# Performance work log

Hardware: AMD Instinct MI355X
Metric: run time of the kernel (lower is better)

Reference implementation:

```python
import jax, jax.numpy as jnp
import numpy as np

MAXHD = 100.0
MAXV = 40.0
LSTM_UNITS = 20
IN_DIM = 12


def setup_inputs() -> dict:
    key = jax.random.key(0)
    ks = jax.random.split(key, 10)
    nveh, nt = 8192, 512
    leadfol_inputs = jax.random.normal(ks[0], (nveh, nt, IN_DIM), dtype=jnp.float32)
    true_traj = jax.random.normal(ks[1], (nveh, nt), dtype=jnp.float32)
    hidden_states = jnp.zeros((2, nveh, LSTM_UNITS), dtype=jnp.float32)
    s = 0.1
    # LSTM kernel/recurrent kernel/bias (keras gate order: i, f, c, o)
    W_k = jax.random.normal(ks[2], (IN_DIM, 4 * LSTM_UNITS), dtype=jnp.float32) * s
    W_r = jax.random.normal(ks[3], (LSTM_UNITS, 4 * LSTM_UNITS), dtype=jnp.float32) * s
    b_l = jnp.zeros((4 * LSTM_UNITS,), dtype=jnp.float32)
    # dense (10, relu) and lc_actions (3)
    W_d = jax.random.normal(ks[4], (LSTM_UNITS, 10), dtype=jnp.float32) * s
    b_d = jnp.zeros((10,), dtype=jnp.float32)
    W_lc = jax.random.normal(ks[5], (10, 3), dtype=jnp.float32) * s
    b_lc = jnp.zeros((3,), dtype=jnp.float32)
    return {"leadfol_inputs": leadfol_inputs, "true_traj": true_traj,
            "hidden_states": hidden_states, "W_k": W_k, "W_r": W_r, "b_l": b_l,
            "W_d": W_d, "b_d": b_d, "W_lc": W_lc, "b_lc": b_lc}


def reference(leadfol_inputs, true_traj, hidden_states, W_k, W_r, b_l, W_d, b_d, W_lc, b_lc):
    # time-major for scan: (nt, nveh, ...)
    lf_t = jnp.swapaxes(leadfol_inputs, 0, 1)
    pos_t = jnp.swapaxes(true_traj, 0, 1)

    def step(carry, xt):
        h, c = carry
        pos, lf = xt  # pos: (nveh,), lf: (nveh, 12)
        lead_hd = (lf[:, :3] - pos[:, None]) / MAXHD
        fol_hd = (pos[:, None] - lf[:, 3:6]) / MAXHD
        spds = lf[:, 6:] / MAXV
        x = jnp.concatenate([lead_hd, fol_hd, spds], axis=1)
        x = jnp.where(jnp.isnan(x), jnp.ones_like(x), x)
        z = x @ W_k + h @ W_r + b_l
        zi, zf, zg, zo = jnp.split(z, 4, axis=1)
        c = jax.nn.sigmoid(zf) * c + jax.nn.sigmoid(zi) * jnp.tanh(zg)
        h = jax.nn.sigmoid(zo) * jnp.tanh(c)
        d = jax.nn.relu(h @ W_d + b_d)
        lc = d @ W_lc + b_lc
        return (h, c), lc

    (h, c), lc_t = jax.lax.scan(step, (hidden_states[0], hidden_states[1]), (pos_t, lf_t))
    pred_lc_action = jnp.swapaxes(lc_t, 0, 1)  # (nveh, nt, 3)
    return (true_traj, pred_lc_action, h, c)
```

## Files before the change

### kernel.cpp

```cpp
#include <hip/hip_runtime.h>

#define NVEH 8192
#define NT   512

typedef short bf16x8 __attribute__((ext_vector_type(8)));
typedef float f32x4  __attribute__((ext_vector_type(4)));

__device__ __forceinline__ float fsig(float x) {
    float e = __builtin_amdgcn_exp2f(-1.44269504f * x);
    return __builtin_amdgcn_rcpf(1.0f + e);
}
__device__ __forceinline__ float ftanh(float x) {
    float e = __builtin_amdgcn_exp2f(-2.88539008f * x);
    return 2.0f * __builtin_amdgcn_rcpf(1.0f + e) - 1.0f;
}
__device__ __forceinline__ unsigned short f2bf(float f) {
    union { float f; unsigned u; } vv; vv.f = f;
    unsigned r = vv.u + 0x7fff + ((vv.u >> 16) & 1);
    return (unsigned short)(r >> 16);
}

__device__ __forceinline__ void lds_barrier() {
    asm volatile("s_waitcnt lgkmcnt(0)" ::: "memory");
    __builtin_amdgcn_s_barrier();
    asm volatile("" ::: "memory");
}

__global__ __launch_bounds__(128) void lstm_scan_kernel(
    const float* __restrict__ lead, const float* __restrict__ traj,
    const float* __restrict__ hidden,
    const float* __restrict__ W_k, const float* __restrict__ W_r,
    const float* __restrict__ b_l, const float* __restrict__ W_d,
    const float* __restrict__ b_d, const float* __restrict__ W_lc,
    const float* __restrict__ b_lc,
    float* __restrict__ out_lc, float* __restrict__ out_h, float* __restrict__ out_c)
{
    __shared__ alignas(16) unsigned short row[2][16][40];

    const int tid  = threadIdx.x;
    const int wid  = tid >> 6;
    const int lane = tid & 63;
    const int q    = lane >> 4;
    const int v    = lane & 15;
    const int gv   = blockIdx.x * 16 + v;

    const int TTB = wid ? 3 : 0;

    bf16x8 aW[3]; f32x4 cB[3];
    #pragma unroll
    for (int l = 0; l < 3; ++l) {
        if (l < 2 || wid == 0) {
            const int tt = TTB + l;
            #pragma unroll
            for (int j = 0; j < 8; ++j) {
                int k = q * 8 + j;
                int p = 16 * tt + v;
                int u = p >> 2, g = p & 3;
                int col = g * 20 + u;
                float w = (k < 12) ? W_k[k * 80 + col] : W_r[(k - 12) * 80 + col];
                aW[l][j] = (short)f2bf(w);
            }
            #pragma unroll
            for (int reg = 0; reg < 4; ++reg)
                cB[l][reg] = b_l[reg * 20 + 4 * tt + q];
        }
    }

    bf16x8 aH = {};
    f32x4 cD = {};
    float wlc[4][3] = {};
    float pb0[3] = {};
    if (wid == 1) {
        #pragma unroll
        for (int j = 0; j < 8; ++j) {
            int k = q * 8 + j;
            aH[j] = (v < 10 && k >= 12) ? (short)f2bf(W_d[(k - 12) * 10 + v]) : (short)0;
        }
        #pragma unroll
        for (int reg = 0; reg < 4; ++reg) {
            int m = 4 * q + reg;
            cD[reg] = (m < 10) ? b_d[m] : 0.0f;
            #pragma unroll
            for (int j = 0; j < 3; ++j)
                wlc[reg][j] = (m < 10) ? W_lc[m * 3 + j] : 0.0f;
        }
        #pragma unroll
        for (int j = 0; j < 3; ++j) pb0[j] = (q == 0) ? b_lc[j] : 0.0f;
    }

    float h32[3], cst[3];
    #pragma unroll
    for (int l = 0; l < 3; ++l) {
        if (l < 2 || wid == 0) {
            int u = 4 * (TTB + l) + q;
            h32[l] = hidden[(size_t)gv * 20 + u];
            cst[l] = hidden[(size_t)NVEH * 20 + (size_t)gv * 20 + u];
            row[1][v][12 + u] = f2bf(h32[l]);
        }
    }

    float Ac[4], Bc[4];
    #pragma unroll
    for (int i = 0; i < 4; ++i) {
        int e = 4 * q + i;
        if (e < 3)      { Ac[i] =  0.01f;  Bc[i] = -0.01f; }
        else if (e < 6) { Ac[i] = -0.01f;  Bc[i] =  0.01f; }
        else            { Ac[i] =  0.025f; Bc[i] =  0.0f;  }
    }

    const float* lf = lead + (size_t)gv * NT * 12;
    const float* ps = traj + (size_t)gv * NT;
    float* lcout    = out_lc + (size_t)gv * NT * 3;

    float4 rA = make_float4(0.f,0.f,0.f,0.f), rB = rA, rC = rA;
    float pA = 0.f, pB = 0.f, pC = 0.f;
    if (wid == 0) {
        float4 r0 = make_float4(0.f,0.f,0.f,0.f); float p0s = 0.f;
        if (q < 3) r0 = *(const float4*)(lf + q * 4);
        if (q < 2) p0s = ps[0];
        if (q < 3) {
            float xv[4] = { r0.x, r0.y, r0.z, r0.w };
            #pragma unroll
            for (int i = 0; i < 4; ++i) {
                float x = fmaf(xv[i], Ac[i], p0s * Bc[i]);
                xv[i] = (x == x) ? x : 1.0f;
            }
            unsigned pk0 = (unsigned)f2bf(xv[0]) | ((unsigned)f2bf(xv[1]) << 16);
            unsigned pk1 = (unsigned)f2bf(xv[2]) | ((unsigned)f2bf(xv[3]) << 16);
            *(uint2*)&row[1][v][4 * q] = make_uint2(pk0, pk1);
        }
        if (q < 3) {
            rA = *(const float4*)(lf + 12 * 1 + q * 4);
            rB = *(const float4*)(lf + 12 * 2 + q * 4);
            rC = *(const float4*)(lf + 12 * 3 + q * 4);
        }
        if (q < 2) { pA = ps[1]; pB = ps[2]; pC = ps[3]; }
    }

    lds_barrier();
    bf16x8 bx = *(const bf16x8*)&row[1][v][8 * q];

    for (int t = 0; t < NT; ++t) {
        if (wid == 0) {
            if (q < 3) {
                float xv[4] = { rA.x, rA.y, rA.z, rA.w };
                #pragma unroll
                for (int i = 0; i < 4; ++i) {
                    float x = fmaf(xv[i], Ac[i], pA * Bc[i]);
                    xv[i] = (x == x) ? x : 1.0f;
                }
                unsigned pk0 = (unsigned)f2bf(xv[0]) | ((unsigned)f2bf(xv[1]) << 16);
                unsigned pk1 = (unsigned)f2bf(xv[2]) | ((unsigned)f2bf(xv[3]) << 16);
                *(uint2*)&row[t & 1][v][4 * q] = make_uint2(pk0, pk1);
            }
            rA = rB; rB = rC; pA = pB; pB = pC;
            int tn = (t + 4 < NT) ? (t + 4) : (NT - 1);
            if (q < 3) rC = *(const float4*)(lf + 12 * tn + q * 4);
            if (q < 2) pC = ps[tn];
        }

        f32x4 z[3];
        z[0] = __builtin_amdgcn_mfma_f32_16x16x32_bf16(aW[0], bx, cB[0], 0, 0, 0);
        z[1] = __builtin_amdgcn_mfma_f32_16x16x32_bf16(aW[1], bx, cB[1], 0, 0, 0);
        if (wid == 0)
            z[2] = __builtin_amdgcn_mfma_f32_16x16x32_bf16(aW[2], bx, cB[2], 0, 0, 0);

        #pragma unroll
        for (int l = 0; l < 3; ++l) {
            if (l < 2 || wid == 0) {
                float si = fsig(z[l][0]);
                float sf = fsig(z[l][1]);
                float tg = ftanh(z[l][2]);
                float so = fsig(z[l][3]);
                float cn = fmaf(sf, cst[l], si * tg);
                cst[l] = cn;
                h32[l] = so * ftanh(cn);
                row[t & 1][v][12 + 4 * (TTB + l) + q] = f2bf(h32[l]);
            }
        }

        lds_barrier();
        bf16x8 bxn = *(const bf16x8*)&row[t & 1][v][8 * q];

        if (wid == 1) {
            f32x4 d = __builtin_amdgcn_mfma_f32_16x16x32_bf16(aH, bxn, cD, 0, 0, 0);
            float dr[4];
            #pragma unroll
            for (int reg = 0; reg < 4; ++reg) dr[reg] = fmaxf(d[reg], 0.0f);
            float p[3];
            #pragma unroll
            for (int j = 0; j < 3; ++j) {
                float acc = pb0[j];
                #pragma unroll
                for (int reg = 0; reg < 4; ++reg) acc = fmaf(dr[reg], wlc[reg][j], acc);
                acc += __shfl_xor(acc, 16);
                acc += __shfl_xor(acc, 32);
                p[j] = acc;
            }
            if (q == (t & 3)) {
                float* o = lcout + (size_t)t * 3;
                *(float2*)o = make_float2(p[0], p[1]);
                o[2] = p[2];
            }
        }
        bx = bxn;
    }

    #pragma unroll
    for (int l = 0; l < 3; ++l) {
        if (l < 2 || wid == 0) {
            int u = 4 * (TTB + l) + q;
            out_h[(size_t)gv * 20 + u] = h32[l];
            out_c[(size_t)gv * 20 + u] = cst[l];
        }
    }
}

extern "C" void kernel_launch(void* const* d_in, const int* in_sizes, int n_in,
                              void* d_out, int out_size, void* d_ws, size_t ws_size,
                              hipStream_t stream) {
    const float* lead   = (const float*)d_in[0];
    const float* traj   = (const float*)d_in[1];
    const float* hidden = (const float*)d_in[2];
    const float* W_k    = (const float*)d_in[3];
    const float* W_r    = (const float*)d_in[4];
    const float* b_l    = (const float*)d_in[5];
    const float* W_d    = (const float*)d_in[6];
    const float* b_d    = (const float*)d_in[7];
    const float* W_lc   = (const float*)d_in[8];
    const float* b_lc   = (const float*)d_in[9];

    float* out    = (float*)d_out;
    float* out_tt = out;
    float* out_lc = out + (size_t)NVEH * NT;
    float* out_h  = out_lc + (size_t)NVEH * NT * 3;
    float* out_c  = out_h + (size_t)NVEH * 20;

    hipMemcpyAsync(out_tt, traj, (size_t)NVEH * NT * sizeof(float),
                   hipMemcpyDeviceToDevice, stream);

    lstm_scan_kernel<<<dim3(NVEH / 16), dim3(128), 0, stream>>>(
        lead, traj, hidden, W_k, W_r, b_l, W_d, b_d, W_lc, b_lc,
        out_lc, out_h, out_c);
}
```

Measured before the change: 722.0 us.

## Split LSTM gate tiles across four waves with dedicated input/output wave

The block grows from two waves to four. Three waves now share the five gate MFMA tiles (2,2,1), and a fourth wave is dedicated to the dense/lc head and to staging the next step's input row. This shortens the serial per-step critical path, since each compute wave does at most two gate tiles and no input preparation. The hidden units are remapped so that one wave writes its h values as a packed pair. Input prefetch depth grows by one step. The cost is more waves per block, which may lower occupancy, and barrier synchronisation across four waves on every step.

After: 657.6 us. 8.9% less time.

```diff
diff --git a/kernel.cpp b/kernel.cpp
--- a/kernel.cpp
+++ b/kernel.cpp
@@ -26,7 +26,7 @@
     asm volatile("" ::: "memory");
 }
 
-__global__ __launch_bounds__(128) void lstm_scan_kernel(
+__global__ __launch_bounds__(256) void lstm_scan_kernel(
     const float* __restrict__ lead, const float* __restrict__ traj,
     const float* __restrict__ hidden,
     const float* __restrict__ W_k, const float* __restrict__ W_r,
@@ -44,33 +44,50 @@
     const int v    = lane & 15;
     const int gv   = blockIdx.x * 16 + v;
 
-    const int TTB = wid ? 3 : 0;
-
-    bf16x8 aW[3]; f32x4 cB[3];
+    const int ntile = (wid < 2) ? 2 : (wid == 2) ? 1 : 0;
+
+    bf16x8 aW[2]; f32x4 cB[2];
+    float h32[2], cst[2];
+    int uu[2];
     #pragma unroll
-    for (int l = 0; l < 3; ++l) {
-        if (l < 2 || wid == 0) {
-            const int tt = TTB + l;
+    for (int l = 0; l < 2; ++l) {
+        if (l < ntile) {
+            const int tt = 2 * wid + l;
             #pragma unroll
             for (int j = 0; j < 8; ++j) {
-                int k = q * 8 + j;
-                int p = 16 * tt + v;
-                int u = p >> 2, g = p & 3;
-                int col = g * 20 + u;
+                int k  = q * 8 + j;
+                int qv = v >> 2, rv = v & 3;
+                int u  = (tt < 4) ? (8 * (tt >> 1) + 2 * qv + (tt & 1)) : (16 + qv);
+                int col = rv * 20 + u;
                 float w = (k < 12) ? W_k[k * 80 + col] : W_r[(k - 12) * 80 + col];
                 aW[l][j] = (short)f2bf(w);
             }
+            uu[l] = (tt < 4) ? (8 * (tt >> 1) + 2 * q + (tt & 1)) : (16 + q);
             #pragma unroll
             for (int reg = 0; reg < 4; ++reg)
-                cB[l][reg] = b_l[reg * 20 + 4 * tt + q];
-        }
-    }
-
-    bf16x8 aH = {};
-    f32x4 cD = {};
-    float wlc[4][3] = {};
-    float pb0[3] = {};
-    if (wid == 1) {
+                cB[l][reg] = b_l[reg * 20 + uu[l]];
+            h32[l] = hidden[(size_t)gv * 20 + uu[l]];
+            cst[l] = hidden[(size_t)NVEH * 20 + (size_t)gv * 20 + uu[l]];
+        }
+    }
+
+    if (wid < 2) {
+        unsigned pk = (unsigned)f2bf(h32[0]) | ((unsigned)f2bf(h32[1]) << 16);
+        *(unsigned*)&row[0][v][12 + 8 * wid + 2 * q] = pk;
+    } else if (wid == 2) {
+        row[0][v][28 + q] = f2bf(h32[0]);
+    }
+
+    const float* lf = lead + (size_t)gv * NT * 12;
+    const float* ps = traj + (size_t)gv * NT;
+    float* lcout    = out_lc + (size_t)gv * NT * 3;
+
+    bf16x8 aH = {}; f32x4 cD = {};
+    float wlc[4][3] = {}; float pb0[3] = {};
+    float Ac[4], Bc[4];
+    float4 rA = make_float4(0.f,0.f,0.f,0.f), rB = rA, rC = rA;
+    float pA = 0.f, pB = 0.f, pC = 0.f;
+    if (wid == 3) {
         #pragma unroll
         for (int j = 0; j < 8; ++j) {
             int k = q * 8 + j;
@@ -86,62 +103,103 @@
         }
         #pragma unroll
         for (int j = 0; j < 3; ++j) pb0[j] = (q == 0) ? b_lc[j] : 0.0f;
-    }
-
-    float h32[3], cst[3];
-    #pragma unroll
-    for (int l = 0; l < 3; ++l) {
-        if (l < 2 || wid == 0) {
-            int u = 4 * (TTB + l) + q;
-            h32[l] = hidden[(size_t)gv * 20 + u];
-            cst[l] = hidden[(size_t)NVEH * 20 + (size_t)gv * 20 + u];
-            row[1][v][12 + u] = f2bf(h32[l]);
-        }
-    }
-
-    float Ac[4], Bc[4];
-    #pragma unroll
-    for (int i = 0; i < 4; ++i) {
-        int e = 4 * q + i;
-        if (e < 3)      { Ac[i] =  0.01f;  Bc[i] = -0.01f; }
-        else if (e < 6) { Ac[i] = -0.01f;  Bc[i] =  0.01f; }
-        else            { Ac[i] =  0.025f; Bc[i] =  0.0f;  }
-    }
-
-    const float* lf = lead + (size_t)gv * NT * 12;
-    const float* ps = traj + (size_t)gv * NT;
-    float* lcout    = out_lc + (size_t)gv * NT * 3;
-
-    float4 rA = make_float4(0.f,0.f,0.f,0.f), rB = rA, rC = rA;
-    float pA = 0.f, pB = 0.f, pC = 0.f;
-    if (wid == 0) {
-        float4 r0 = make_float4(0.f,0.f,0.f,0.f); float p0s = 0.f;
-        if (q < 3) r0 = *(const float4*)(lf + q * 4);
-        if (q < 2) p0s = ps[0];
+
+        #pragma unroll
+        for (int i = 0; i < 4; ++i) {
+            int e = 4 * q + i;
+            if (e < 3)      { Ac[i] =  0.01f;  Bc[i] = -0.01f; }
+            else if (e < 6) { Ac[i] = -0.01f;  Bc[i] =  0.01f; }
+            else            { Ac[i] =  0.025f; Bc[i] =  0.0f;  }
+        }
+
+        #pragma unroll
+        for (int s = 0; s < 2; ++s) {
+            float4 r0 = make_float4(0.f,0.f,0.f,0.f); float p0s = 0.f;
+            if (q < 3) r0 = *(const float4*)(lf + 12 * s + q * 4);
+            if (q < 2) p0s = ps[s];
+            if (q < 3) {
+                float xv[4] = { r0.x, r0.y, r0.z, r0.w };
+                #pragma unroll
+                for (int i = 0; i < 4; ++i) {
+                    float x = fmaf(xv[i], Ac[i], p0s * Bc[i]);
+                    xv[i] = (x == x) ? x : 1.0f;
+                }
+                unsigned pk0 = (unsigned)f2bf(xv[0]) | ((unsigned)f2bf(xv[1]) << 16);
+                unsigned pk1 = (unsigned)f2bf(xv[2]) | ((unsigned)f2bf(xv[3]) << 16);
+                *(uint2*)&row[s][v][4 * q] = make_uint2(pk0, pk1);
+            }
+        }
         if (q < 3) {
-            float xv[4] = { r0.x, r0.y, r0.z, r0.w };
-            #pragma unroll
-            for (int i = 0; i < 4; ++i) {
-                float x = fmaf(xv[i], Ac[i], p0s * Bc[i]);
-                xv[i] = (x == x) ? x : 1.0f;
-            }
-            unsigned pk0 = (unsigned)f2bf(xv[0]) | ((unsigned)f2bf(xv[1]) << 16);
-            unsigned pk1 = (unsigned)f2bf(xv[2]) | ((unsigned)f2bf(xv[3]) << 16);
-            *(uint2*)&row[1][v][4 * q] = make_uint2(pk0, pk1);
-        }
-        if (q < 3) {
-            rA = *(const float4*)(lf + 12 * 1 + q * 4);
-            rB = *(const float4*)(lf + 12 * 2 + q * 4);
-            rC = *(const float4*)(lf + 12 * 3 + q * 4);
-        }
-        if (q < 2) { pA = ps[1]; pB = ps[2]; pC = ps[3]; }
+            rA = *(const float4*)(lf + 12 * 2 + q * 4);
+            rB = *(const float4*)(lf + 12 * 3 + q * 4);
+            rC = *(const float4*)(lf + 12 * 4 + q * 4);
+        }
+        if (q < 2) { pA = ps[2]; pB = ps[3]; pC = ps[4]; }
     }
 
     lds_barrier();
-    bf16x8 bx = *(const bf16x8*)&row[1][v][8 * q];
+    bf16x8 bx = *(const bf16x8*)&row[0][v][8 * q];
 
     for (int t = 0; t < NT; ++t) {
-        if (wid == 0) {
+        const int nxt = (t + 1) & 1;
+
+        if (wid < 3) {
+            f32x4 z0 = __builtin_amdgcn_mfma_f32_16x16x32_bf16(aW[0], bx, cB[0], 0, 0, 0);
+            f32x4 z1;
+            if (ntile == 2)
+                z1 = __builtin_amdgcn_mfma_f32_16x16x32_bf16(aW[1], bx, cB[1], 0, 0, 0);
+
+            {
+                float si = fsig(z0[0]);
+                float sf = fsig(z0[1]);
+                float tg = ftanh(z0[2]);
+                float so = fsig(z0[3]);
+                float cn = fmaf(sf, cst[0], si * tg);
+                cst[0] = cn;
+                h32[0] = so * ftanh(cn);
+            }
+            if (ntile == 2) {
+                float si = fsig(z1[0]);
+                float sf = fsig(z1[1]);
+                float tg = ftanh(z1[2]);
+                float so = fsig(z1[3]);
+                float cn = fmaf(sf, cst[1], si * tg);
+                cst[1] = cn;
+                h32[1] = so * ftanh(cn);
+            }
+
+            if (wid < 2) {
+                unsigned pk = (unsigned)f2bf(h32[0]) | ((unsigned)f2bf(h32[1]) << 16);
+                *(unsigned*)&row[nxt][v][12 + 8 * wid + 2 * q] = pk;
+            } else {
+                row[nxt][v][28 + q] = f2bf(h32[0]);
+            }
+        }
+
+        lds_barrier();
+        bf16x8 bxn = *(const bf16x8*)&row[nxt][v][8 * q];
+
+        if (wid == 3) {
+            f32x4 d = __builtin_amdgcn_mfma_f32_16x16x32_bf16(aH, bxn, cD, 0, 0, 0);
+            float dr[4];
+            #pragma unroll
+            for (int reg = 0; reg < 4; ++reg) dr[reg] = fmaxf(d[reg], 0.0f);
+            float p[3];
+            #pragma unroll
+            for (int j = 0; j < 3; ++j) {
+                float acc = pb0[j];
+                #pragma unroll
+                for (int reg = 0; reg < 4; ++reg) acc = fmaf(dr[reg], wlc[reg][j], acc);
+                acc += __shfl_xor(acc, 16);
+                acc += __shfl_xor(acc, 32);
+                p[j] = acc;
+            }
+            if (q == (t & 3)) {
+                float* o = lcout + (size_t)t * 3;
+                *(float2*)o = make_float2(p[0], p[1]);
+                o[2] = p[2];
+            }
+
             if (q < 3) {
                 float xv[4] = { rA.x, rA.y, rA.z, rA.w };
                 #pragma unroll
@@ -154,64 +212,21 @@
                 *(uint2*)&row[t & 1][v][4 * q] = make_uint2(pk0, pk1);
             }
             rA = rB; rB = rC; pA = pB; pB = pC;
-            int tn = (t + 4 < NT) ? (t + 4) : (NT - 1);
+            int tn = (t + 5 < NT) ? (t + 5) : (NT - 1);
             if (q < 3) rC = *(const float4*)(lf + 12 * tn + q * 4);
             if (q < 2) pC = ps[tn];
         }
 
-        f32x4 z[3];
-        z[0] = __builtin_amdgcn_mfma_f32_16x16x32_bf16(aW[0], bx, cB[0], 0, 0, 0);
-        z[1] = __builtin_amdgcn_mfma_f32_16x16x32_bf16(aW[1], bx, cB[1], 0, 0, 0);
-        if (wid == 0)
-            z[2] = __builtin_amdgcn_mfma_f32_16x16x32_bf16(aW[2], bx, cB[2], 0, 0, 0);
-
-        #pragma unroll
-        for (int l = 0; l < 3; ++l) {
-            if (l < 2 || wid == 0) {
-                float si = fsig(z[l][0]);
-                float sf = fsig(z[l][1]);
-                float tg = ftanh(z[l][2]);
-                float so = fsig(z[l][3]);
-                float cn = fmaf(sf, cst[l], si * tg);
-                cst[l] = cn;
-                h32[l] = so * ftanh(cn);
-                row[t & 1][v][12 + 4 * (TTB + l) + q] = f2bf(h32[l]);
-            }
-        }
-
-        lds_barrier();
-        bf16x8 bxn = *(const bf16x8*)&row[t & 1][v][8 * q];
-
-        if (wid == 1) {
-            f32x4 d = __builtin_amdgcn_mfma_f32_16x16x32_bf16(aH, bxn, cD, 0, 0, 0);
-            float dr[4];
-            #pragma unroll
-            for (int reg = 0; reg < 4; ++reg) dr[reg] = fmaxf(d[reg], 0.0f);
-            float p[3];
-            #pragma unroll
-            for (int j = 0; j < 3; ++j) {
-                float acc = pb0[j];
-                #pragma unroll
-                for (int reg = 0; reg < 4; ++reg) acc = fmaf(dr[reg], wlc[reg][j], acc);
-                acc += __shfl_xor(acc, 16);
-                acc += __shfl_xor(acc, 32);
-                p[j] = acc;
-            }
-            if (q == (t & 3)) {
-                float* o = lcout + (size_t)t * 3;
-                *(float2*)o = make_float2(p[0], p[1]);
-                o[2] = p[2];
-            }
-        }
         bx = bxn;
     }
 
-    #pragma unroll
-    for (int l = 0; l < 3; ++l) {
-        if (l < 2 || wid == 0) {
-            int u = 4 * (TTB + l) + q;
-            out_h[(size_t)gv * 20 + u] = h32[l];
-            out_c[(size_t)gv * 20 + u] = cst[l];
+    if (wid < 3) {
+        #pragma unroll
+        for (int l = 0; l < 2; ++l) {
+            if (l < ntile) {
+                out_h[(size_t)gv * 20 + uu[l]] = h32[l];
+                out_c[(size_t)gv * 20 + uu[l]] = cst[l];
+            }
         }
     }
 }
@@ -239,7 +254,7 @@
     hipMemcpyAsync(out_tt, traj, (size_t)NVEH * NT * sizeof(float),
                    hipMemcpyDeviceToDevice, stream);
 
-    lstm_scan_kernel<<<dim3(NVEH / 16), dim3(128), 0, stream>>>(
+    lstm_scan_kernel<<<dim3(NVEH / 16), dim3(256), 0, stream>>>(
         lead, traj, hidden, W_k, W_r, b_l, W_d, b_d, W_lc, b_lc,
         out_lc, out_h, out_c);
 }
```
